# Optimization experiments

Measured on AMD Instinct MI355X. Metric: run time of the kernel, lower is better.

Reference implementation:

```python
import jax, jax.numpy as jnp
import numpy as np

B, L, D = 2, 4096, 128      # batch, seq_len, d_model
ED = 2 * D                  # d_inner (expand=2) = 256
N = 16                      # d_state
K = 4                       # d_conv
R = (D + 15) // 16          # dt_rank = 8
H = 2 * D                   # mlp hidden = 256


def setup_inputs() -> dict:
    key = jax.random.key(0)
    ks = jax.random.split(key, 20)
    s = 0.05
    inp = {
        "x": jax.random.normal(ks[0], (B, L, D), dtype=jnp.float32),
        # outer block LayerNorm (norm1)
        "norm1_g": jnp.ones((D,), jnp.float32),
        "norm1_b": jnp.zeros((D,), jnp.float32),
        # MambaLayer inner LayerNorm
        "inner_g": jnp.ones((D,), jnp.float32),
        "inner_b": jnp.zeros((D,), jnp.float32),
        # Mamba params
        "in_w": jax.random.normal(ks[1], (2 * ED, D), jnp.float32) * s,      # in_proj (no bias)
        "conv_w": jax.random.normal(ks[2], (ED, 1, K), jnp.float32) * s,     # depthwise conv
        "conv_b": jax.random.normal(ks[3], (ED,), jnp.float32) * s,
        "xproj_w": jax.random.normal(ks[4], (R + 2 * N, ED), jnp.float32) * s,  # x_proj (no bias)
        "dt_w": jax.random.normal(ks[5], (ED, R), jnp.float32) * s,
        "dt_b": jax.random.normal(ks[6], (ED,), jnp.float32) * s,
        "A_log": jnp.tile(jnp.log(jnp.arange(1, N + 1, dtype=jnp.float32)), (ED, 1)),  # [ED,N]
        "Dp": jnp.ones((ED,), jnp.float32),
        "out_w": jax.random.normal(ks[7], (D, ED), jnp.float32) * s,         # out_proj (no bias)
        # MLP
        "fc1_w": jax.random.normal(ks[8], (H, D), jnp.float32) * s,
        "fc1_b": jnp.zeros((H,), jnp.float32),
        "fc2_w": jax.random.normal(ks[9], (D, H), jnp.float32) * s,
        "fc2_b": jnp.zeros((D,), jnp.float32),
    }
    return inp


def _ln(x, g, b, eps=1e-5):
    m = jnp.mean(x, axis=-1, keepdims=True)
    v = jnp.mean((x - m) ** 2, axis=-1, keepdims=True)
    return (x - m) * jax.lax.rsqrt(v + eps) * g + b


def _mamba(x, in_w, conv_w, conv_b, xproj_w, dt_w, dt_b, A_log, Dp, out_w):
    # x: [B, L, D]
    xz = jnp.einsum('bld,ed->ble', x, in_w)          # [B,L,2*ED]
    u, z = jnp.split(xz, 2, axis=-1)                 # each [B,L,ED]
    # causal depthwise conv1d over L
    u_c = jnp.transpose(u, (0, 2, 1))                # [B,ED,L]
    u_c = jax.lax.conv_general_dilated(
        u_c, conv_w, window_strides=(1,), padding=[(K - 1, 0)],
        dimension_numbers=('NCH', 'OIH', 'NCH'), feature_group_count=ED)
    u = jax.nn.silu(jnp.transpose(u_c, (0, 2, 1)) + conv_b)   # [B,L,ED]
    # input-dependent dt, B, C
    dbc = jnp.einsum('ble,re->blr', u, xproj_w)      # [B,L,R+2N]
    dt, Bm, Cm = jnp.split(dbc, [R, R + N], axis=-1)
    delta = jax.nn.softplus(jnp.einsum('blr,er->ble', dt, dt_w) + dt_b)  # [B,L,ED]
    A = -jnp.exp(A_log)                              # [ED,N]
    deltaA = jnp.exp(jnp.einsum('ble,en->blen', delta, A))               # [B,L,ED,N]
    deltaBu = jnp.einsum('ble,bln,ble->blen', delta, Bm, u)              # [B,L,ED,N]
    # selective scan over L
    def step(h, inp):
        dA, dBu, Ct = inp                            # [B,ED,N],[B,ED,N],[B,N]
        h = dA * h + dBu
        y = jnp.einsum('ben,bn->be', h, Ct)
        return h, y
    h0 = jnp.zeros((B, ED, N), u.dtype)
    xs = (jnp.transpose(deltaA, (1, 0, 2, 3)),
          jnp.transpose(deltaBu, (1, 0, 2, 3)),
          jnp.transpose(Cm, (1, 0, 2)))
    _, ys = jax.lax.scan(step, h0, xs)               # [L,B,ED]
    y = jnp.transpose(ys, (1, 0, 2)) + u * Dp        # [B,L,ED]
    y = y * jax.nn.silu(z)
    return jnp.einsum('ble,de->bld', y, out_w)       # [B,L,D]


def reference(x, norm1_g, norm1_b, inner_g, inner_b, in_w, conv_w, conv_b,
              xproj_w, dt_w, dt_b, A_log, Dp, out_w, fc1_w, fc1_b, fc2_w, fc2_b):
    # attn branch: mamba(inner_LN(norm1(x)))
    a = _mamba(_ln(_ln(x, norm1_g, norm1_b), inner_g, inner_b),
               in_w, conv_w, conv_b, xproj_w, dt_w, dt_b, A_log, Dp, out_w)
    x = x + a
    # mlp branch (note: original applies norm1 again to updated x)
    h = _ln(x, norm1_g, norm1_b)
    h = jax.nn.gelu(jnp.einsum('bld,hd->blh', h, fc1_w) + fc1_b, approximate=False)
    h = jnp.einsum('blh,dh->bld', h, fc2_w) + fc2_b
    return x + h
```

## Files before the change

kernel.cpp:

```cpp
#include <hip/hip_runtime.h>
#include <hip/hip_bf16.h>
#include <math.h>

#define BB 2
#define LL 4096
#define DD 128
#define ED 256
#define NN 16
#define KK 4
#define RR 8
#define HH 256
#define NT (BB*LL)
#define NC 128
#define LC 32

#define LOG2E 1.4426950408889634f

typedef __attribute__((ext_vector_type(8))) short short8;
typedef __attribute__((ext_vector_type(8))) unsigned short ushort8v;
typedef __attribute__((ext_vector_type(4))) float floatx4;

__device__ __forceinline__ unsigned short f2bf(float f) {
  unsigned int b = __builtin_bit_cast(unsigned int, f);
  b += 0x7FFFu + ((b >> 16) & 1u);
  return (unsigned short)(b >> 16);
}

__device__ __forceinline__ float exp2_fast(float x) {
#if __has_builtin(__builtin_amdgcn_exp2f)
  return __builtin_amdgcn_exp2f(x);
#else
  return exp2f(x);
#endif
}

__device__ __forceinline__ ushort8v pack8(const float4& v0, const float4& v1) {
  ushort8v p;
  p[0]=f2bf(v0.x); p[1]=f2bf(v0.y); p[2]=f2bf(v0.z); p[3]=f2bf(v0.w);
  p[4]=f2bf(v1.x); p[5]=f2bf(v1.y); p[6]=f2bf(v1.z); p[7]=f2bf(v1.w);
  return p;
}

__global__ __launch_bounds__(256) void gemm_inln_k(const float* __restrict__ x,
    const float* __restrict__ g1, const float* __restrict__ b1,
    const float* __restrict__ g2, const float* __restrict__ b2,
    const float* __restrict__ W, float* __restrict__ C) {
  __shared__ unsigned short As[64][136];
  __shared__ unsigned short Ws[64][136];
  const int row0 = blockIdx.y * 64;
  const int col0 = blockIdx.x * 64;
  const int tid  = threadIdx.x;
  const int wave = tid >> 6, lane = tid & 63;
  const int quad = lane >> 4, l16 = lane & 15;
  const int wm = (wave & 1) * 32, wn = (wave >> 1) * 32;
  const int lr = tid >> 2;
  const int lk = (tid & 3) * 32;

  {
    const float* Ap = x + (size_t)(row0 + lr)*DD + lk;
    float4 av[8];
    float s = 0.f, sq = 0.f;
    #pragma unroll
    for (int g = 0; g < 8; g++) {
      av[g] = *(const float4*)(Ap + g*4);
      s  += av[g].x + av[g].y + av[g].z + av[g].w;
      sq += av[g].x*av[g].x + av[g].y*av[g].y + av[g].z*av[g].z + av[g].w*av[g].w;
    }
    s += __shfl_xor(s, 1);  s += __shfl_xor(s, 2);
    sq += __shfl_xor(sq, 1); sq += __shfl_xor(sq, 2);
    const float m1 = s * (1.f/128.f);
    const float rs1 = rsqrtf(sq*(1.f/128.f) - m1*m1 + 1e-5f);
    float s2 = 0.f, sq2 = 0.f;
    #pragma unroll
    for (int g = 0; g < 8; g++) {
      const float4 gg = *(const float4*)(g1 + lk + g*4);
      const float4 bb = *(const float4*)(b1 + lk + g*4);
      av[g].x = (av[g].x - m1)*rs1*gg.x + bb.x;
      av[g].y = (av[g].y - m1)*rs1*gg.y + bb.y;
      av[g].z = (av[g].z - m1)*rs1*gg.z + bb.z;
      av[g].w = (av[g].w - m1)*rs1*gg.w + bb.w;
      s2  += av[g].x + av[g].y + av[g].z + av[g].w;
      sq2 += av[g].x*av[g].x + av[g].y*av[g].y + av[g].z*av[g].z + av[g].w*av[g].w;
    }
    s2 += __shfl_xor(s2, 1);  s2 += __shfl_xor(s2, 2);
    sq2 += __shfl_xor(sq2, 1); sq2 += __shfl_xor(sq2, 2);
    const float m2 = s2 * (1.f/128.f);
    const float rs2 = rsqrtf(sq2*(1.f/128.f) - m2*m2 + 1e-5f);
    #pragma unroll
    for (int g = 0; g < 4; g++) {
      const float4 ga = *(const float4*)(g2 + lk + g*8);
      const float4 gb = *(const float4*)(g2 + lk + g*8 + 4);
      const float4 ba = *(const float4*)(b2 + lk + g*8);
      const float4 bbv= *(const float4*)(b2 + lk + g*8 + 4);
      ushort8v pa;
      pa[0] = f2bf((av[2*g].x   - m2)*rs2*ga.x + ba.x);
      pa[1] = f2bf((av[2*g].y   - m2)*rs2*ga.y + ba.y);
      pa[2] = f2bf((av[2*g].z   - m2)*rs2*ga.z + ba.z);
      pa[3] = f2bf((av[2*g].w   - m2)*rs2*ga.w + ba.w);
      pa[4] = f2bf((av[2*g+1].x - m2)*rs2*gb.x + bbv.x);
      pa[5] = f2bf((av[2*g+1].y - m2)*rs2*gb.y + bbv.y);
      pa[6] = f2bf((av[2*g+1].z - m2)*rs2*gb.z + bbv.z);
      pa[7] = f2bf((av[2*g+1].w - m2)*rs2*gb.w + bbv.w);
      *(ushort8v*)&As[lr][lk + g*8] = pa;
    }
  }
  {
    const float* Wp = W + (size_t)(col0 + lr)*DD + lk;
    #pragma unroll
    for (int g = 0; g < 4; g++) {
      const float4 v0 = *(const float4*)(Wp + g*8);
      const float4 v1 = *(const float4*)(Wp + g*8 + 4);
      *(ushort8v*)&Ws[lr][lk + g*8] = pack8(v0, v1);
    }
  }
  __syncthreads();

  floatx4 acc[2][2] = {};
  #pragma unroll
  for (int ks = 0; ks < 4; ks++) {
    const int ko = ks*32 + quad*8;
    short8 a0 = *(const short8*)&As[wm +      l16][ko];
    short8 a1 = *(const short8*)&As[wm + 16 + l16][ko];
    short8 b0 = *(const short8*)&Ws[wn +      l16][ko];
    short8 b1 = *(const short8*)&Ws[wn + 16 + l16][ko];
    acc[0][0] = __builtin_amdgcn_mfma_f32_16x16x32_bf16(a0, b0, acc[0][0], 0, 0, 0);
    acc[0][1] = __builtin_amdgcn_mfma_f32_16x16x32_bf16(a0, b1, acc[0][1], 0, 0, 0);
    acc[1][0] = __builtin_amdgcn_mfma_f32_16x16x32_bf16(a1, b0, acc[1][0], 0, 0, 0);
    acc[1][1] = __builtin_amdgcn_mfma_f32_16x16x32_bf16(a1, b1, acc[1][1], 0, 0, 0);
  }
  #pragma unroll
  for (int i = 0; i < 2; i++)
    #pragma unroll
    for (int j = 0; j < 2; j++) {
      const int n = col0 + wn + j*16 + l16;
      #pragma unroll
      for (int r = 0; r < 4; r++) {
        const int m = row0 + wm + i*16 + quad*4 + r;
        C[(size_t)m*(2*ED) + n] = acc[i][j][r];
      }
    }
}

__global__ __launch_bounds__(256) void scan1f_k(
    const float* __restrict__ xz, const float* __restrict__ cw,
    const float* __restrict__ cb, const float* __restrict__ xpw,
    const float* __restrict__ dtw, const float* __restrict__ dtb,
    const float* __restrict__ A_log, float* __restrict__ uc,
    float* __restrict__ dbc, float* __restrict__ delta,
    float* __restrict__ cA, float* __restrict__ cH) {
  __shared__ __align__(16) unsigned short Bs[64][264];
  __shared__ __align__(16) unsigned short As[32][264];
  __shared__ float su[32][128];
  __shared__ float sdbc[32][40];
  float (*sdel)[128] = reinterpret_cast<float(*)[128]>(&As[0][0]);

  const int eb = blockIdx.x, c = blockIdx.y, b = blockIdx.z;
  const int tid = threadIdx.x;
  const int t0 = b*LL + c*LC;

  #pragma unroll
  for (int p = 0; p < 8; p++) {
    const int idx = p*256 + tid;
    const int row = idx >> 5;
    const int col = (idx & 31) * 8;
    ushort8v v = {};
    if (row < 40) {
      const float4 v0 = *(const float4*)(xpw + (size_t)row*ED + col);
      const float4 v1 = *(const float4*)(xpw + (size_t)row*ED + col + 4);
      v = pack8(v0, v1);
    }
    *(ushort8v*)&Bs[row][col] = v;
  }

  {
    const int ch = tid;
    const float4 w = *(const float4*)(cw + ch*4);
    const float cbe = cb[ch];
    float xv[32];
    #pragma unroll
    for (int i = 0; i < LC; i++)
      xv[i] = xz[(size_t)(t0+i)*(2*ED) + ch];
    float h0 = 0.f, h1 = 0.f, h2 = 0.f;
    if (c != 0) {
      h0 = xz[(size_t)(t0-3)*(2*ED) + ch];
      h1 = xz[(size_t)(t0-2)*(2*ED) + ch];
      h2 = xz[(size_t)(t0-1)*(2*ED) + ch];
    }
    const bool own = (ch >> 7) == eb;
    #pragma unroll
    for (int i = 0; i < LC; i++) {
      const float cur = xv[i];
      const float a = cbe + h0*w.x + h1*w.y + h2*w.z + cur*w.w;
      const float s = a / (1.f + __expf(-a));
      As[i][ch] = f2bf(s);
      if (own) {
        su[i][ch & 127] = s;
        uc[(size_t)(t0+i)*ED + ch] = s;
      }
      h0 = h1; h1 = h2; h2 = cur;
    }
  }
  __syncthreads();

  const int wave = tid >> 6, lane = tid & 63;
  const int quad = lane >> 4, l16 = lane & 15;
  {
    const int mi = (wave & 1) * 16;
    const int j0 = (wave >> 1) * 2;
    floatx4 acc[2] = {};
    #pragma unroll
    for (int ks = 0; ks < 8; ks++) {
      const int ko = ks*32 + quad*8;
      short8 a  = *(const short8*)&As[mi + l16][ko];
      short8 b0 = *(const short8*)&Bs[j0*16 +      l16][ko];
      short8 b1 = *(const short8*)&Bs[j0*16 + 16 + l16][ko];
      acc[0] = __builtin_amdgcn_mfma_f32_16x16x32_bf16(a, b0, acc[0], 0, 0, 0);
      acc[1] = __builtin_amdgcn_mfma_f32_16x16x32_bf16(a, b1, acc[1], 0, 0, 0);
    }
    __syncthreads();
    #pragma unroll
    for (int f = 0; f < 2; f++) {
      const int n = (j0 + f)*16 + l16;
      #pragma unroll
      for (int r = 0; r < 4; r++) {
        const int m = mi + quad*4 + r;
        if (n < 40) {
          sdbc[m][n] = acc[f][r];
          if (eb == 0) dbc[(size_t)(t0 + m)*40 + n] = acc[f][r];
        }
      }
    }
  }
  __syncthreads();

  const int e_loc = tid >> 1;
  const int half  = tid & 1;
  const int e     = eb*128 + e_loc;
  {
    const float4 w0 = *(const float4*)(dtw + e*RR);
    const float4 w1 = *(const float4*)(dtw + e*RR + 4);
    const float db = dtb[e];
    #pragma unroll 4
    for (int i = 0; i < 16; i++) {
      const int t = half*16 + i;
      const float a = db
          + sdbc[t][0]*w0.x + sdbc[t][1]*w0.y + sdbc[t][2]*w0.z + sdbc[t][3]*w0.w
          + sdbc[t][4]*w1.x + sdbc[t][5]*w1.y + sdbc[t][6]*w1.z + sdbc[t][7]*w1.w;
      const float d = (a > 20.f) ? a : log1pf(__expf(a));
      sdel[t][e_loc] = d;
      delta[(size_t)(t0+t)*ED + e] = d;
    }
  }
  __syncthreads();

  const int n0 = half * 8;
  const float4 a0 = *(const float4*)(A_log + e*NN + n0);
  const float4 a1 = *(const float4*)(A_log + e*NN + n0 + 4);
  float Aen[8] = {-__expf(a0.x)*LOG2E, -__expf(a0.y)*LOG2E,
                  -__expf(a0.z)*LOG2E, -__expf(a0.w)*LOG2E,
                  -__expf(a1.x)*LOG2E, -__expf(a1.y)*LOG2E,
                  -__expf(a1.z)*LOG2E, -__expf(a1.w)*LOG2E};
  float h[8] = {};
  float sumd = 0.f;
  for (int i = 0; i < LC; i++) {
    const float dv = sdel[i][e_loc];
    const float du = dv * su[i][e_loc];
    const float4 B0 = *(const float4*)&sdbc[i][RR + n0];
    const float4 B1 = *(const float4*)&sdbc[i][RR + n0 + 4];
    const float Bv[8] = {B0.x,B0.y,B0.z,B0.w,B1.x,B1.y,B1.z,B1.w};
    sumd += dv;
    #pragma unroll
    for (int j = 0; j < 8; j++)
      h[j] = exp2_fast(dv * Aen[j])*h[j] + Bv[j]*du;
  }
  const size_t base = (((size_t)c*BB + b)*ED + e)*NN + n0;
  *(float4*)(cA + base)     = make_float4(exp2_fast(sumd*Aen[0]), exp2_fast(sumd*Aen[1]),
                                          exp2_fast(sumd*Aen[2]), exp2_fast(sumd*Aen[3]));
  *(float4*)(cA + base + 4) = make_float4(exp2_fast(sumd*Aen[4]), exp2_fast(sumd*Aen[5]),
                                          exp2_fast(sumd*Aen[6]), exp2_fast(sumd*Aen[7]));
  *(float4*)(cH + base)     = make_float4(h[0], h[1], h[2], h[3]);
  *(float4*)(cH + base + 4) = make_float4(h[4], h[5], h[6], h[7]);
}

__global__ __launch_bounds__(64) void scan2_k(float* __restrict__ cA,
    const float* __restrict__ cH) {
  const int gt = blockIdx.x*64 + threadIdx.x;
  const int b = gt >> 12;
  const size_t base = (size_t)b*ED*NN + (gt & 4095);
  float h = 0.f;
  for (int g = 0; g < NC/16; g++) {
    float av[16], hv[16];
    #pragma unroll
    for (int i = 0; i < 16; i++) {
      const size_t idx = (size_t)(g*16 + i)*(BB*ED*NN) + base;
      av[i] = cA[idx]; hv[i] = cH[idx];
    }
    #pragma unroll
    for (int i = 0; i < 16; i++) {
      const size_t idx = (size_t)(g*16 + i)*(BB*ED*NN) + base;
      cA[idx] = h;
      h = av[i]*h + hv[i];
    }
  }
}

__global__ __launch_bounds__(512, 1) void tail5_k(
    const float* __restrict__ xz, const float* __restrict__ delta,
    const float* __restrict__ uc, const float* __restrict__ dbc,
    const float* __restrict__ cP, const float* __restrict__ A_log,
    const float* __restrict__ Dpv, const float* __restrict__ x,
    const float* __restrict__ g1, const float* __restrict__ b1,
    const float* __restrict__ out_w, const float* __restrict__ fc1_w,
    const float* __restrict__ fc1_b, const float* __restrict__ fc2_w,
    const float* __restrict__ fc2_b, float* __restrict__ out) {
  __shared__ __align__(16) unsigned short BigW[34816];
  __shared__ __align__(16) unsigned short Au[32][264];
  __shared__ float xs[32][132];
  __shared__ float sbc[32][32];

  const int c = blockIdx.x, b = blockIdx.y;
  const int t0 = b*LL + c*LC;
  const int tid = threadIdx.x;
  const int wave = tid >> 6, lane = tid & 63;
  const int quad = lane >> 4, l16 = lane & 15;

  if (tid < 256) {
    const int row = tid >> 3, c4 = (tid & 7) * 4;
    *(float4*)&sbc[row][c4] = *(const float4*)(dbc + (size_t)(t0 + row)*40 + RR + c4);
  }
  __syncthreads();

  {
    const int r = tid >> 2, k0 = (tid & 3) * 64;
    const float* wp = out_w + (size_t)r*ED + k0;
    #pragma unroll
    for (int g = 0; g < 8; g++) {
      const float4 v0 = *(const float4*)(wp + g*8);
      const float4 v1 = *(const float4*)(wp + g*8 + 4);
      *(ushort8v*)&BigW[(size_t)r*264 + k0 + g*8] = pack8(v0, v1);
    }
  }

  {
    const int e = tid >> 1, half = tid & 1;
    const int n0 = half * 8;
    float Aen[8], h[8];
    {
      const float4 a0 = *(const float4*)(A_log + e*NN + n0);
      const float4 a1 = *(const float4*)(A_log + e*NN + n0 + 4);
      Aen[0]=-__expf(a0.x)*LOG2E; Aen[1]=-__expf(a0.y)*LOG2E;
      Aen[2]=-__expf(a0.z)*LOG2E; Aen[3]=-__expf(a0.w)*LOG2E;
      Aen[4]=-__expf(a1.x)*LOG2E; Aen[5]=-__expf(a1.y)*LOG2E;
      Aen[6]=-__expf(a1.z)*LOG2E; Aen[7]=-__expf(a1.w)*LOG2E;
      const size_t pb = (((size_t)c*BB + b)*ED + e)*NN + n0;
      const float4 h0 = *(const float4*)(cP + pb);
      const float4 h1 = *(const float4*)(cP + pb + 4);
      h[0]=h0.x; h[1]=h0.y; h[2]=h0.z; h[3]=h0.w;
      h[4]=h1.x; h[5]=h1.y; h[6]=h1.z; h[7]=h1.w;
    }
    const float Dpe = Dpv[e];
    float pd[8], pu[8], pz[8];
    #pragma unroll
    for (int i = 0; i < 8; i++) {
      pd[i] = delta[(size_t)(t0+i)*ED + e];
      pu[i] = uc[(size_t)(t0+i)*ED + e];
      pz[i] = xz[(size_t)(t0+i)*(2*ED) + ED + e];
    }
    for (int g4 = 0; g4 < 4; g4++) {
      float cd[8], cu[8], cz[8];
      #pragma unroll
      for (int i = 0; i < 8; i++) { cd[i]=pd[i]; cu[i]=pu[i]; cz[i]=pz[i]; }
      if (g4 < 3) {
        const int tn = t0 + (g4+1)*8;
        #pragma unroll
        for (int i = 0; i < 8; i++) {
          pd[i] = delta[(size_t)(tn+i)*ED + e];
          pu[i] = uc[(size_t)(tn+i)*ED + e];
          pz[i] = xz[(size_t)(tn+i)*(2*ED) + ED + e];
        }
      }
      #pragma unroll
      for (int i = 0; i < 8; i++) {
        const int t = g4*8 + i;
        const float dv = cd[i];
        const float uv = cu[i];
        const float du = dv * uv;
        const float4 B0 = *(const float4*)&sbc[t][n0];
        const float4 B1 = *(const float4*)&sbc[t][n0 + 4];
        const float4 C0 = *(const float4*)&sbc[t][16 + n0];
        const float4 C1 = *(const float4*)&sbc[t][16 + n0 + 4];
        const float Bv[8] = {B0.x,B0.y,B0.z,B0.w, B1.x,B1.y,B1.z,B1.w};
        const float Cv[8] = {C0.x,C0.y,C0.z,C0.w, C1.x,C1.y,C1.z,C1.w};
        float part = 0.f;
        #pragma unroll
        for (int j = 0; j < 8; j++) {
          h[j] = exp2_fast(dv * Aen[j])*h[j] + Bv[j]*du;
          part += h[j]*Cv[j];
        }
        part += __shfl_xor(part, 1);
        if (half == 0) {
          const float g = cz[i] / (1.f + __expf(-cz[i]));
          Au[t][e] = f2bf((part + uv*Dpe) * g);
        }
      }
    }
  }
  __syncthreads();

  {
    const int wn = wave * 16;
    floatx4 acc[2] = {};
    #pragma unroll
    for (int ks = 0; ks < 8; ks++) {
      const int ko = ks*32 + quad*8;
      short8 a0 = *(const short8*)&Au[l16][ko];
      short8 a1 = *(const short8*)&Au[16 + l16][ko];
      short8 bv = *(const short8*)&BigW[(size_t)(wn + l16)*264 + ko];
      acc[0] = __builtin_amdgcn_mfma_f32_16x16x32_bf16(a0, bv, acc[0], 0, 0, 0);
      acc[1] = __builtin_amdgcn_mfma_f32_16x16x32_bf16(a1, bv, acc[1], 0, 0, 0);
    }
    #pragma unroll
    for (int i = 0; i < 2; i++) {
      const int n = wn + l16;
      #pragma unroll
      for (int r = 0; r < 4; r++) {
        const int m = i*16 + quad*4 + r;
        xs[m][n] = acc[i][r] + x[(size_t)(t0 + m)*DD + n];
      }
    }
  }
  __syncthreads();

  {
    const int lr = tid >> 4, le = (tid & 15) * 8;
    float vv[8];
    float s = 0.f, sq = 0.f;
    #pragma unroll
    for (int i = 0; i < 8; i++) {
      vv[i] = xs[lr][le + i];
      s += vv[i]; sq += vv[i]*vv[i];
    }
    s += __shfl_xor(s, 1);  s += __shfl_xor(s, 2);
    s += __shfl_xor(s, 4);  s += __shfl_xor(s, 8);
    sq += __shfl_xor(sq, 1); sq += __shfl_xor(sq, 2);
    sq += __shfl_xor(sq, 4); sq += __shfl_xor(sq, 8);
    const float mean = s * (1.f/128.f);
    const float rs = rsqrtf(sq*(1.f/128.f) - mean*mean + 1e-5f);
    ushort8v p;
    #pragma unroll
    for (int i = 0; i < 8; i++)
      p[i] = f2bf((vv[i] - mean)*rs*g1[le + i] + b1[le + i]);
    *(ushort8v*)&Au[lr][le] = p;
  }
  {
    const int r = tid >> 1, k0 = (tid & 1) * 64;
    const float* wp = fc1_w + (size_t)r*DD + k0;
    #pragma unroll
    for (int g = 0; g < 8; g++) {
      const float4 v0 = *(const float4*)(wp + g*8);
      const float4 v1 = *(const float4*)(wp + g*8 + 4);
      *(ushort8v*)&BigW[(size_t)r*136 + k0 + g*8] = pack8(v0, v1);
    }
  }
  __syncthreads();

  {
    const int wn = wave * 32;
    floatx4 acc[2][2] = {};
    #pragma unroll
    for (int ks = 0; ks < 4; ks++) {
      const int ko = ks*32 + quad*8;
      short8 a0 = *(const short8*)&Au[l16][ko];
      short8 a1 = *(const short8*)&Au[16 + l16][ko];
      short8 b0 = *(const short8*)&BigW[(size_t)(wn +      l16)*136 + ko];
      short8 b1 = *(const short8*)&BigW[(size_t)(wn + 16 + l16)*136 + ko];
      acc[0][0] = __builtin_amdgcn_mfma_f32_16x16x32_bf16(a0, b0, acc[0][0], 0, 0, 0);
      acc[0][1] = __builtin_amdgcn_mfma_f32_16x16x32_bf16(a0, b1, acc[0][1], 0, 0, 0);
      acc[1][0] = __builtin_amdgcn_mfma_f32_16x16x32_bf16(a1, b0, acc[1][0], 0, 0, 0);
      acc[1][1] = __builtin_amdgcn_mfma_f32_16x16x32_bf16(a1, b1, acc[1][1], 0, 0, 0);
    }
    __syncthreads();
    #pragma unroll
    for (int i = 0; i < 2; i++)
      #pragma unroll
      for (int f = 0; f < 2; f++) {
        const int n = wn + f*16 + l16;
        const float bn = fc1_b[n];
        #pragma unroll
        for (int r = 0; r < 4; r++) {
          const int m = i*16 + quad*4 + r;
          float v = acc[i][f][r] + bn;
          v = 0.5f*v*(1.f + erff(v*0.70710678118f));
          Au[m][n] = f2bf(v);
        }
      }
  }
  {
    const int r = tid >> 2, k0 = (tid & 3) * 64;
    const float* wp = fc2_w + (size_t)r*HH + k0;
    __syncthreads();
    #pragma unroll
    for (int g = 0; g < 8; g++) {
      const float4 v0 = *(const float4*)(wp + g*8);
      const float4 v1 = *(const float4*)(wp + g*8 + 4);
      *(ushort8v*)&BigW[(size_t)r*264 + k0 + g*8] = pack8(v0, v1);
    }
  }
  __syncthreads();

  {
    const int wn = wave * 16;
    floatx4 acc[2] = {};
    #pragma unroll
    for (int ks = 0; ks < 8; ks++) {
      const int ko = ks*32 + quad*8;
      short8 a0 = *(const short8*)&Au[l16][ko];
      short8 a1 = *(const short8*)&Au[16 + l16][ko];
      short8 bv = *(const short8*)&BigW[(size_t)(wn + l16)*264 + ko];
      acc[0] = __builtin_amdgcn_mfma_f32_16x16x32_bf16(a0, bv, acc[0], 0, 0, 0);
      acc[1] = __builtin_amdgcn_mfma_f32_16x16x32_bf16(a1, bv, acc[1], 0, 0, 0);
    }
    #pragma unroll
    for (int i = 0; i < 2; i++) {
      const int n = wn + l16;
      const float bn = fc2_b[n];
      #pragma unroll
      for (int r = 0; r < 4; r++) {
        const int m = i*16 + quad*4 + r;
        out[(size_t)(t0 + m)*DD + n] = acc[i][r] + bn + xs[m][n];
      }
    }
  }
}

extern "C" void kernel_launch(void* const* d_in, const int* in_sizes, int n_in,
                              void* d_out, int out_size, void* d_ws, size_t ws_size,
                              hipStream_t stream) {
  const float* x      = (const float*)d_in[0];
  const float* n1g    = (const float*)d_in[1];
  const float* n1b    = (const float*)d_in[2];
  const float* ing    = (const float*)d_in[3];
  const float* inb    = (const float*)d_in[4];
  const float* in_w   = (const float*)d_in[5];
  const float* conv_w = (const float*)d_in[6];
  const float* conv_b = (const float*)d_in[7];
  const float* xproj_w= (const float*)d_in[8];
  const float* dt_w   = (const float*)d_in[9];
  const float* dt_b   = (const float*)d_in[10];
  const float* A_log  = (const float*)d_in[11];
  const float* Dpv    = (const float*)d_in[12];
  const float* out_w  = (const float*)d_in[13];
  const float* fc1_w  = (const float*)d_in[14];
  const float* fc1_b  = (const float*)d_in[15];
  const float* fc2_w  = (const float*)d_in[16];
  const float* fc2_b  = (const float*)d_in[17];
  float* out = (float*)d_out;

  float* ws    = (float*)d_ws;
  float* xz    = ws;
  float* uc    = xz    + (size_t)NT*2*ED;
  float* dbc   = uc    + (size_t)NT*ED;
  float* delta = dbc   + (size_t)NT*40;
  float* cAP   = delta + (size_t)NT*ED;
  float* cH    = cAP   + (size_t)NC*BB*ED*NN;

  gemm_inln_k<<<dim3(512/64, NT/64), 256, 0, stream>>>(x, n1g, n1b, ing, inb, in_w, xz);
  scan1f_k<<<dim3(2, NC, BB), 256, 0, stream>>>(xz, conv_w, conv_b, xproj_w, dt_w, dt_b,
                                                A_log, uc, dbc, delta, cAP, cH);
  scan2_k<<<(BB*ED*NN)/64, 64, 0, stream>>>(cAP, cH);
  tail5_k<<<dim3(NC, BB), 512, 0, stream>>>(xz, delta, uc, dbc, cAP, A_log, Dpv,
                                            x, n1g, n1b, out_w, fc1_w, fc1_b,
                                            fc2_w, fc2_b, out);
}
```

Baseline: 174.6 us.

## Fuse double LayerNorm and in_proj GEMM into the chunk scan kernel

```diff
diff --git a/kernel.cpp b/kernel.cpp
--- a/kernel.cpp
+++ b/kernel.cpp
@@ -41,122 +41,161 @@
   return p;
 }
 
-__global__ __launch_bounds__(256) void gemm_inln_k(const float* __restrict__ x,
+__global__ __launch_bounds__(256) void scan1g_k(
+    const float* __restrict__ x,
     const float* __restrict__ g1, const float* __restrict__ b1,
     const float* __restrict__ g2, const float* __restrict__ b2,
-    const float* __restrict__ W, float* __restrict__ C) {
-  __shared__ unsigned short As[64][136];
-  __shared__ unsigned short Ws[64][136];
-  const int row0 = blockIdx.y * 64;
-  const int col0 = blockIdx.x * 64;
-  const int tid  = threadIdx.x;
-  const int wave = tid >> 6, lane = tid & 63;
-  const int quad = lane >> 4, l16 = lane & 15;
-  const int wm = (wave & 1) * 32, wn = (wave >> 1) * 32;
-  const int lr = tid >> 2;
-  const int lk = (tid & 3) * 32;
-
-  {
-    const float* Ap = x + (size_t)(row0 + lr)*DD + lk;
-    float4 av[8];
-    float s = 0.f, sq = 0.f;
-    #pragma unroll
-    for (int g = 0; g < 8; g++) {
-      av[g] = *(const float4*)(Ap + g*4);
-      s  += av[g].x + av[g].y + av[g].z + av[g].w;
-      sq += av[g].x*av[g].x + av[g].y*av[g].y + av[g].z*av[g].z + av[g].w*av[g].w;
-    }
-    s += __shfl_xor(s, 1);  s += __shfl_xor(s, 2);
-    sq += __shfl_xor(sq, 1); sq += __shfl_xor(sq, 2);
-    const float m1 = s * (1.f/128.f);
-    const float rs1 = rsqrtf(sq*(1.f/128.f) - m1*m1 + 1e-5f);
-    float s2 = 0.f, sq2 = 0.f;
-    #pragma unroll
-    for (int g = 0; g < 8; g++) {
-      const float4 gg = *(const float4*)(g1 + lk + g*4);
-      const float4 bb = *(const float4*)(b1 + lk + g*4);
-      av[g].x = (av[g].x - m1)*rs1*gg.x + bb.x;
-      av[g].y = (av[g].y - m1)*rs1*gg.y + bb.y;
-      av[g].z = (av[g].z - m1)*rs1*gg.z + bb.z;
-      av[g].w = (av[g].w - m1)*rs1*gg.w + bb.w;
-      s2  += av[g].x + av[g].y + av[g].z + av[g].w;
-      sq2 += av[g].x*av[g].x + av[g].y*av[g].y + av[g].z*av[g].z + av[g].w*av[g].w;
-    }
-    s2 += __shfl_xor(s2, 1);  s2 += __shfl_xor(s2, 2);
-    sq2 += __shfl_xor(sq2, 1); sq2 += __shfl_xor(sq2, 2);
-    const float m2 = s2 * (1.f/128.f);
-    const float rs2 = rsqrtf(sq2*(1.f/128.f) - m2*m2 + 1e-5f);
-    #pragma unroll
-    for (int g = 0; g < 4; g++) {
-      const float4 ga = *(const float4*)(g2 + lk + g*8);
-      const float4 gb = *(const float4*)(g2 + lk + g*8 + 4);
-      const float4 ba = *(const float4*)(b2 + lk + g*8);
-      const float4 bbv= *(const float4*)(b2 + lk + g*8 + 4);
-      ushort8v pa;
-      pa[0] = f2bf((av[2*g].x   - m2)*rs2*ga.x + ba.x);
-      pa[1] = f2bf((av[2*g].y   - m2)*rs2*ga.y + ba.y);
-      pa[2] = f2bf((av[2*g].z   - m2)*rs2*ga.z + ba.z);
-      pa[3] = f2bf((av[2*g].w   - m2)*rs2*ga.w + ba.w);
-      pa[4] = f2bf((av[2*g+1].x - m2)*rs2*gb.x + bbv.x);
-      pa[5] = f2bf((av[2*g+1].y - m2)*rs2*gb.y + bbv.y);
-      pa[6] = f2bf((av[2*g+1].z - m2)*rs2*gb.z + bbv.z);
-      pa[7] = f2bf((av[2*g+1].w - m2)*rs2*gb.w + bbv.w);
-      *(ushort8v*)&As[lr][lk + g*8] = pa;
-    }
-  }
-  {
-    const float* Wp = W + (size_t)(col0 + lr)*DD + lk;
-    #pragma unroll
-    for (int g = 0; g < 4; g++) {
-      const float4 v0 = *(const float4*)(Wp + g*8);
-      const float4 v1 = *(const float4*)(Wp + g*8 + 4);
-      *(ushort8v*)&Ws[lr][lk + g*8] = pack8(v0, v1);
-    }
-  }
-  __syncthreads();
-
-  floatx4 acc[2][2] = {};
-  #pragma unroll
-  for (int ks = 0; ks < 4; ks++) {
-    const int ko = ks*32 + quad*8;
-    short8 a0 = *(const short8*)&As[wm +      l16][ko];
-    short8 a1 = *(const short8*)&As[wm + 16 + l16][ko];
-    short8 b0 = *(const short8*)&Ws[wn +      l16][ko];
-    short8 b1 = *(const short8*)&Ws[wn + 16 + l16][ko];
-    acc[0][0] = __builtin_amdgcn_mfma_f32_16x16x32_bf16(a0, b0, acc[0][0], 0, 0, 0);
-    acc[0][1] = __builtin_amdgcn_mfma_f32_16x16x32_bf16(a0, b1, acc[0][1], 0, 0, 0);
-    acc[1][0] = __builtin_amdgcn_mfma_f32_16x16x32_bf16(a1, b0, acc[1][0], 0, 0, 0);
-    acc[1][1] = __builtin_amdgcn_mfma_f32_16x16x32_bf16(a1, b1, acc[1][1], 0, 0, 0);
-  }
-  #pragma unroll
-  for (int i = 0; i < 2; i++)
-    #pragma unroll
-    for (int j = 0; j < 2; j++) {
-      const int n = col0 + wn + j*16 + l16;
-      #pragma unroll
-      for (int r = 0; r < 4; r++) {
-        const int m = row0 + wm + i*16 + quad*4 + r;
-        C[(size_t)m*(2*ED) + n] = acc[i][j][r];
-      }
-    }
-}
-
-__global__ __launch_bounds__(256) void scan1f_k(
-    const float* __restrict__ xz, const float* __restrict__ cw,
-    const float* __restrict__ cb, const float* __restrict__ xpw,
+    const float* __restrict__ in_w,
+    const float* __restrict__ cw, const float* __restrict__ cb,
+    const float* __restrict__ xpw,
     const float* __restrict__ dtw, const float* __restrict__ dtb,
-    const float* __restrict__ A_log, float* __restrict__ uc,
-    float* __restrict__ dbc, float* __restrict__ delta,
+    const float* __restrict__ A_log,
+    float* __restrict__ uc, float* __restrict__ dbc,
+    float* __restrict__ delta, float* __restrict__ gate,
     float* __restrict__ cA, float* __restrict__ cH) {
-  __shared__ __align__(16) unsigned short Bs[64][264];
-  __shared__ __align__(16) unsigned short As[32][264];
-  __shared__ float su[32][128];
-  __shared__ float sdbc[32][40];
-  float (*sdel)[128] = reinterpret_cast<float(*)[128]>(&As[0][0]);
+  __shared__ __align__(16) unsigned char SM[69776];
+  auto Atile = reinterpret_cast<unsigned short(*)[136]>(SM);
+  auto Wch   = reinterpret_cast<unsigned short(*)[136]>(SM);
+  auto As    = reinterpret_cast<unsigned short(*)[264]>(SM);
+  auto sdel  = reinterpret_cast<float(*)[128]>(SM);
+  auto ubuf  = reinterpret_cast<float(*)[257]>(SM + 17408);
+  auto Bs    = reinterpret_cast<unsigned short(*)[264]>(SM + 17408);
+  auto sdbc  = reinterpret_cast<float(*)[40]>(SM + 17408);
+  auto sus   = reinterpret_cast<float(*)[128]>(SM + 53392);
 
   const int eb = blockIdx.x, c = blockIdx.y, b = blockIdx.z;
   const int tid = threadIdx.x;
   const int t0 = b*LL + c*LC;
+  const int wave = tid >> 6, lane = tid & 63;
+  const int quad = lane >> 4, l16 = lane & 15;
+
+  {
+    const int lr = tid >> 2, lk = (tid & 3) * 32;
+    if (lr < 48) {
+      if (lr < 35 && !(c == 0 && lr < 3)) {
+        const float* Ap = x + (size_t)(t0 - 3 + lr)*DD + lk;
+        float4 av[8];
+        float s = 0.f, sq = 0.f;
+        #pragma unroll
+        for (int g = 0; g < 8; g++) {
+          av[g] = *(const float4*)(Ap + g*4);
+          s  += av[g].x + av[g].y + av[g].z + av[g].w;
+          sq += av[g].x*av[g].x + av[g].y*av[g].y + av[g].z*av[g].z + av[g].w*av[g].w;
+        }
+        s += __shfl_xor(s, 1);  s += __shfl_xor(s, 2);
+        sq += __shfl_xor(sq, 1); sq += __shfl_xor(sq, 2);
+        const float m1 = s * (1.f/128.f);
+        const float rs1 = rsqrtf(sq*(1.f/128.f) - m1*m1 + 1e-5f);
+        float s2 = 0.f, sq2 = 0.f;
+        #pragma unroll
+        for (int g = 0; g < 8; g++) {
+          const float4 gg = *(const float4*)(g1 + lk + g*4);
+          const float4 bb = *(const float4*)(b1 + lk + g*4);
+          av[g].x = (av[g].x - m1)*rs1*gg.x + bb.x;
+          av[g].y = (av[g].y - m1)*rs1*gg.y + bb.y;
+          av[g].z = (av[g].z - m1)*rs1*gg.z + bb.z;
+          av[g].w = (av[g].w - m1)*rs1*gg.w + bb.w;
+          s2  += av[g].x + av[g].y + av[g].z + av[g].w;
+          sq2 += av[g].x*av[g].x + av[g].y*av[g].y + av[g].z*av[g].z + av[g].w*av[g].w;
+        }
+        s2 += __shfl_xor(s2, 1);  s2 += __shfl_xor(s2, 2);
+        sq2 += __shfl_xor(sq2, 1); sq2 += __shfl_xor(sq2, 2);
+        const float m2 = s2 * (1.f/128.f);
+        const float rs2 = rsqrtf(sq2*(1.f/128.f) - m2*m2 + 1e-5f);
+        #pragma unroll
+        for (int g = 0; g < 4; g++) {
+          const float4 ga = *(const float4*)(g2 + lk + g*8);
+          const float4 gb = *(const float4*)(g2 + lk + g*8 + 4);
+          const float4 ba = *(const float4*)(b2 + lk + g*8);
+          const float4 bbv= *(const float4*)(b2 + lk + g*8 + 4);
+          ushort8v pa;
+          pa[0] = f2bf((av[2*g].x   - m2)*rs2*ga.x + ba.x);
+          pa[1] = f2bf((av[2*g].y   - m2)*rs2*ga.y + ba.y);
+          pa[2] = f2bf((av[2*g].z   - m2)*rs2*ga.z + ba.z);
+          pa[3] = f2bf((av[2*g].w   - m2)*rs2*ga.w + ba.w);
+          pa[4] = f2bf((av[2*g+1].x - m2)*rs2*gb.x + bbv.x);
+          pa[5] = f2bf((av[2*g+1].y - m2)*rs2*gb.y + bbv.y);
+          pa[6] = f2bf((av[2*g+1].z - m2)*rs2*gb.z + bbv.z);
+          pa[7] = f2bf((av[2*g+1].w - m2)*rs2*gb.w + bbv.w);
+          *(ushort8v*)&Atile[lr][lk + g*8] = pa;
+        }
+      } else {
+        const ushort8v zz = {};
+        #pragma unroll
+        for (int g = 0; g < 4; g++) *(ushort8v*)&Atile[lr][lk + g*8] = zz;
+      }
+    }
+  }
+  __syncthreads();
+
+  short8 af[3][4];
+  #pragma unroll
+  for (int mt = 0; mt < 3; mt++)
+    #pragma unroll
+    for (int ks = 0; ks < 4; ks++)
+      af[mt][ks] = *(const short8*)&Atile[mt*16 + l16][ks*32 + quad*8];
+  __syncthreads();
+
+  for (int nc = 0; nc < 6; nc++) {
+    const int colbase = (nc < 4) ? nc*64 : 256 + eb*128 + (nc-4)*64;
+    {
+      const int r = tid >> 2, seg = (tid & 3) * 32;
+      const float* wp = in_w + (size_t)(colbase + r)*DD + seg;
+      #pragma unroll
+      for (int g = 0; g < 4; g++) {
+        const float4 v0 = *(const float4*)(wp + g*8);
+        const float4 v1 = *(const float4*)(wp + g*8 + 4);
+        *(ushort8v*)&Wch[r][seg + g*8] = pack8(v0, v1);
+      }
+    }
+    __syncthreads();
+    floatx4 acc[3] = {};
+    #pragma unroll
+    for (int ks = 0; ks < 4; ks++) {
+      short8 bv = *(const short8*)&Wch[wave*16 + l16][ks*32 + quad*8];
+      #pragma unroll
+      for (int mt = 0; mt < 3; mt++)
+        acc[mt] = __builtin_amdgcn_mfma_f32_16x16x32_bf16(af[mt][ks], bv, acc[mt], 0, 0, 0);
+    }
+    const int coll = wave*16 + l16;
+    #pragma unroll
+    for (int mt = 0; mt < 3; mt++)
+      #pragma unroll
+      for (int rr = 0; rr < 4; rr++) {
+        const int m = mt*16 + quad*4 + rr;
+        if (nc < 4) {
+          if (m < 35) ubuf[m][nc*64 + coll] = acc[mt][rr];
+        } else {
+          if (m >= 3 && m < 35) {
+            const float v = acc[mt][rr];
+            gate[(size_t)(t0 + m - 3)*ED + (colbase - 256) + coll] =
+                v / (1.f + __expf(-v));
+          }
+        }
+      }
+    __syncthreads();
+  }
+
+  {
+    const int ch = tid;
+    const float4 w = *(const float4*)(cw + ch*4);
+    const float cbe = cb[ch];
+    float h0 = ubuf[0][ch], h1 = ubuf[1][ch], h2 = ubuf[2][ch];
+    const bool own = (ch >> 7) == eb;
+    #pragma unroll
+    for (int i = 0; i < LC; i++) {
+      const float cur = ubuf[3+i][ch];
+      const float a = cbe + h0*w.x + h1*w.y + h2*w.z + cur*w.w;
+      const float s = a / (1.f + __expf(-a));
+      As[i][ch] = f2bf(s);
+      if (own) {
+        sus[i][ch & 127] = s;
+        uc[(size_t)(t0+i)*ED + ch] = s;
+      }
+      h0 = h1; h1 = h2; h2 = cur;
+    }
+  }
+  __syncthreads();
 
   #pragma unroll
   for (int p = 0; p < 8; p++) {
@@ -171,39 +210,8 @@
     }
     *(ushort8v*)&Bs[row][col] = v;
   }
-
-  {
-    const int ch = tid;
-    const float4 w = *(const float4*)(cw + ch*4);
-    const float cbe = cb[ch];
-    float xv[32];
-    #pragma unroll
-    for (int i = 0; i < LC; i++)
-      xv[i] = xz[(size_t)(t0+i)*(2*ED) + ch];
-    float h0 = 0.f, h1 = 0.f, h2 = 0.f;
-    if (c != 0) {
-      h0 = xz[(size_t)(t0-3)*(2*ED) + ch];
-      h1 = xz[(size_t)(t0-2)*(2*ED) + ch];
-      h2 = xz[(size_t)(t0-1)*(2*ED) + ch];
-    }
-    const bool own = (ch >> 7) == eb;
-    #pragma unroll
-    for (int i = 0; i < LC; i++) {
-      const float cur = xv[i];
-      const float a = cbe + h0*w.x + h1*w.y + h2*w.z + cur*w.w;
-      const float s = a / (1.f + __expf(-a));
-      As[i][ch] = f2bf(s);
-      if (own) {
-        su[i][ch & 127] = s;
-        uc[(size_t)(t0+i)*ED + ch] = s;
-      }
-      h0 = h1; h1 = h2; h2 = cur;
-    }
-  }
-  __syncthreads();
-
-  const int wave = tid >> 6, lane = tid & 63;
-  const int quad = lane >> 4, l16 = lane & 15;
+  __syncthreads();
+
   {
     const int mi = (wave & 1) * 16;
     const int j0 = (wave >> 1) * 2;
@@ -264,7 +272,7 @@
   float sumd = 0.f;
   for (int i = 0; i < LC; i++) {
     const float dv = sdel[i][e_loc];
-    const float du = dv * su[i][e_loc];
+    const float du = dv * sus[i][e_loc];
     const float4 B0 = *(const float4*)&sdbc[i][RR + n0];
     const float4 B1 = *(const float4*)&sdbc[i][RR + n0 + 4];
     const float Bv[8] = {B0.x,B0.y,B0.z,B0.w,B1.x,B1.y,B1.z,B1.w};
@@ -304,8 +312,8 @@
   }
 }
 
-__global__ __launch_bounds__(512, 1) void tail5_k(
-    const float* __restrict__ xz, const float* __restrict__ delta,
+__global__ __launch_bounds__(512, 1) void tail6_k(
+    const float* __restrict__ gate, const float* __restrict__ delta,
     const float* __restrict__ uc, const float* __restrict__ dbc,
     const float* __restrict__ cP, const float* __restrict__ A_log,
     const float* __restrict__ Dpv, const float* __restrict__ x,
@@ -359,24 +367,24 @@
       h[4]=h1.x; h[5]=h1.y; h[6]=h1.z; h[7]=h1.w;
     }
     const float Dpe = Dpv[e];
-    float pd[8], pu[8], pz[8];
+    float pd[8], pu[8], pg[8];
     #pragma unroll
     for (int i = 0; i < 8; i++) {
       pd[i] = delta[(size_t)(t0+i)*ED + e];
       pu[i] = uc[(size_t)(t0+i)*ED + e];
-      pz[i] = xz[(size_t)(t0+i)*(2*ED) + ED + e];
+      pg[i] = gate[(size_t)(t0+i)*ED + e];
     }
     for (int g4 = 0; g4 < 4; g4++) {
-      float cd[8], cu[8], cz[8];
-      #pragma unroll
-      for (int i = 0; i < 8; i++) { cd[i]=pd[i]; cu[i]=pu[i]; cz[i]=pz[i]; }
+      float cd[8], cu[8], cg[8];
+      #pragma unroll
+      for (int i = 0; i < 8; i++) { cd[i]=pd[i]; cu[i]=pu[i]; cg[i]=pg[i]; }
       if (g4 < 3) {
         const int tn = t0 + (g4+1)*8;
         #pragma unroll
         for (int i = 0; i < 8; i++) {
           pd[i] = delta[(size_t)(tn+i)*ED + e];
           pu[i] = uc[(size_t)(tn+i)*ED + e];
-          pz[i] = xz[(size_t)(tn+i)*(2*ED) + ED + e];
+          pg[i] = gate[(size_t)(tn+i)*ED + e];
         }
       }
       #pragma unroll
@@ -398,10 +406,8 @@
           part += h[j]*Cv[j];
         }
         part += __shfl_xor(part, 1);
-        if (half == 0) {
-          const float g = cz[i] / (1.f + __expf(-cz[i]));
-          Au[t][e] = f2bf((part + uv*Dpe) * g);
-        }
+        if (half == 0)
+          Au[t][e] = f2bf((part + uv*Dpe) * cg[i]);
       }
     }
   }
@@ -557,18 +563,18 @@
   float* out = (float*)d_out;
 
   float* ws    = (float*)d_ws;
-  float* xz    = ws;
-  float* uc    = xz    + (size_t)NT*2*ED;
+  float* uc    = ws;
   float* dbc   = uc    + (size_t)NT*ED;
   float* delta = dbc   + (size_t)NT*40;
-  float* cAP   = delta + (size_t)NT*ED;
-  float* cH    = cAP   + (size_t)NC*BB*ED*NN;
-
-  gemm_inln_k<<<dim3(512/64, NT/64), 256, 0, stream>>>(x, n1g, n1b, ing, inb, in_w, xz);
-  scan1f_k<<<dim3(2, NC, BB), 256, 0, stream>>>(xz, conv_w, conv_b, xproj_w, dt_w, dt_b,
-                                                A_log, uc, dbc, delta, cAP, cH);
-  scan2_k<<<(BB*ED*NN)/64, 64, 0, stream>>>(cAP, cH);
-  tail5_k<<<dim3(NC, BB), 512, 0, stream>>>(xz, delta, uc, dbc, cAP, A_log, Dpv,
+  float* gate  = delta + (size_t)NT*ED;
+  float* cA    = gate  + (size_t)NT*ED;
+  float* cH    = cA    + (size_t)NC*BB*ED*NN;
+
+  scan1g_k<<<dim3(2, NC, BB), 256, 0, stream>>>(x, n1g, n1b, ing, inb, in_w,
+                                                conv_w, conv_b, xproj_w, dt_w, dt_b,
+                                                A_log, uc, dbc, delta, gate, cA, cH);
+  scan2_k<<<(BB*ED*NN)/64, 64, 0, stream>>>(cA, cH);
+  tail6_k<<<dim3(NC, BB), 512, 0, stream>>>(gate, delta, uc, dbc, cA, A_log, Dpv,
                                             x, n1g, n1b, out_w, fc1_w, fc1_b,
                                             fc2_w, fc2_b, out);
 }
```

New measurement: 164.5 us. -5.8%, faster.
